# Optimization experiments

Measured on AMD Instinct MI355X. Metric: run time of the kernel, lower is better.

## Reference

```python
import jax, jax.numpy as jnp
import numpy as np

BT, P, C = 64, 1024, 1024   # bt = B*T with T=8 frames
T = 8
B = BT // T
RANK, DSTATE = 32, 16
SCALING = 128.0 / 32.0      # alpha / rank


def setup_inputs() -> dict:
    key = jax.random.key(0)
    ks = jax.random.split(key, 11)
    s = 0.02
    return {
        "x": jax.random.normal(ks[0], (BT, P, C), jnp.float32),
        "Wb": jax.random.normal(ks[1], (C, C), jnp.float32) * s,
        "bb": jax.random.normal(ks[2], (C,), jnp.float32) * s,
        "Wdown": jax.random.normal(ks[3], (RANK, C), jnp.float32) * s,
        "Wup": jax.random.normal(ks[4], (C, RANK), jnp.float32) * s,
        "A_log": jax.random.normal(ks[5], (RANK, DSTATE), jnp.float32),
        "Dp": jax.random.normal(ks[6], (RANK,), jnp.float32),
        "Wxp": jax.random.normal(ks[7], (RANK + 2 * DSTATE, RANK), jnp.float32) * s,
        "bxp": jnp.zeros((RANK + 2 * DSTATE,), jnp.float32),
        "Wout": jax.random.normal(ks[8], (RANK, RANK), jnp.float32) * s,
        "bout": jnp.zeros((RANK,), jnp.float32),
    }


def _minimal_ssm(xseq, A_log, Dp, Wxp, bxp, Wout, bout):
    # xseq: (N, T, r) -> (N, T, r); serial recurrence over T via lax.scan.
    N, Tn, r = xseq.shape
    A = -jnp.exp(A_log)  # (r, s)

    def step(h, x_t):  # h: (N, r, s), x_t: (N, r)
        proj = x_t @ Wxp.T + bxp                      # (N, r + 2s)
        dlt = jax.nn.softplus(proj[:, :r])            # (N, r)
        Bm = proj[:, r:r + DSTATE]                    # (N, s)
        Cm = proj[:, r + DSTATE:]                     # (N, s)
        A_bar = jnp.exp(dlt[:, :, None] * A)          # (N, r, s)
        B_bar = dlt[:, :, None] * Bm[:, None, :]      # (N, r, s)
        h = A_bar * h + B_bar * x_t[:, :, None]
        y = jnp.einsum('nrs,ns->nr', h, Cm) + Dp * x_t
        return h, y

    h0 = jnp.zeros((N, r, DSTATE), xseq.dtype)
    _, ys = jax.lax.scan(step, h0, jnp.swapaxes(xseq, 0, 1))  # ys: (T, N, r)
    out = jnp.swapaxes(ys, 0, 1)                               # (N, T, r)
    return out @ Wout.T + bout


def reference(x, Wb, bb, Wdown, Wup, A_log, Dp, Wxp, bxp, Wout, bout):
    base_out = x @ Wb.T + bb                                   # (BT, P, C)
    x_btpc = x.reshape(B, T, P, C)
    red = jnp.einsum('btpc,rc->btpr', x_btpc, Wdown)           # (B, T, P, r)
    red_seq = jnp.transpose(red, (0, 2, 1, 3)).reshape(B * P, T, RANK)
    red_seq = _minimal_ssm(red_seq, A_log, Dp, Wxp, bxp, Wout, bout)
    red_seq = jnp.transpose(red_seq.reshape(B, P, T, RANK), (0, 2, 1, 3))
    delta = jnp.einsum('btpr,cr->btpc', red_seq, Wup) * SCALING
    return base_out + delta.reshape(BT, P, C)
```

## Files before the change

### kernel.cpp

```cpp
#include <hip/hip_runtime.h>
#include <stdint.h>

typedef unsigned short u16;
typedef short short8 __attribute__((ext_vector_type(8)));
typedef float f32x4 __attribute__((ext_vector_type(4)));

#define MFMA16(a,b,c) __builtin_amdgcn_mfma_f32_16x16x32_bf16((a),(b),(c),0,0,0)

__device__ __forceinline__ u16 f2bf(float f) {
  union { float f; unsigned u; } v; v.f = f;
  unsigned r = v.u + 0x7FFFu + ((v.u >> 16) & 1u);
  return (u16)(r >> 16);
}

__device__ __forceinline__ void async16(u16* lds, const u16* g) {
  __builtin_amdgcn_global_load_lds(
      (const __attribute__((address_space(1))) void*)g,
      (__attribute__((address_space(3))) void*)lds, 16, 0, 0);
}

__global__ __launch_bounds__(256) void k_conv_w(const float* __restrict__ wb,
                                                const float* __restrict__ wdown,
                                                const float* __restrict__ wup,
                                                u16* __restrict__ wbb,
                                                u16* __restrict__ wdownb,
                                                u16* __restrict__ wupb) {
  int idx = blockIdx.x * blockDim.x + threadIdx.x;
  int total = gridDim.x * blockDim.x;
  for (int i = idx; i < 1024 * 1024 / 8; i += total) {
    const float4* p = (const float4*)(wb + (size_t)i * 8);
    float4 a = p[0], b = p[1];
    union { u16 h[8]; uint4 v; } o;
    o.h[0] = f2bf(a.x); o.h[1] = f2bf(a.y); o.h[2] = f2bf(a.z); o.h[3] = f2bf(a.w);
    o.h[4] = f2bf(b.x); o.h[5] = f2bf(b.y); o.h[6] = f2bf(b.z); o.h[7] = f2bf(b.w);
    *(uint4*)(wbb + (size_t)i * 8) = o.v;
  }
  for (int i = idx; i < 32 * 1024; i += total) wdownb[i] = f2bf(wdown[i]);
  for (int i = idx; i < 1024 * 32; i += total) wupb[i] = f2bf(wup[i] * 4.0f);
}

__global__ __launch_bounds__(256) void k_prep(const float* __restrict__ x,
                                              const u16* __restrict__ wdownb,
                                              u16* __restrict__ xb,
                                              float* __restrict__ red) {
  int lane = threadIdx.x & 63, wid = threadIdx.x >> 6;
  int base = blockIdx.x * 64 + wid * 16;
  int row = base + (lane & 15);
  int q8 = (lane >> 4) * 8;
  const float* gx = x + (size_t)row * 1024 + q8;
  u16* gxb = xb + (size_t)row * 1024 + q8;
  const u16* wd0 = wdownb + (size_t)(lane & 15) * 1024 + q8;
  f32x4 acc0 = {}, acc1 = {};
#pragma unroll 4
  for (int k0 = 0; k0 < 1024; k0 += 32) {
    float4 a = *(const float4*)(gx + k0);
    float4 c = *(const float4*)(gx + k0 + 4);
    union { u16 h[8]; uint4 v; short8 s; } o;
    o.h[0] = f2bf(a.x); o.h[1] = f2bf(a.y); o.h[2] = f2bf(a.z); o.h[3] = f2bf(a.w);
    o.h[4] = f2bf(c.x); o.h[5] = f2bf(c.y); o.h[6] = f2bf(c.z); o.h[7] = f2bf(c.w);
    *(uint4*)(gxb + k0) = o.v;
    short8 b0 = *(const short8*)(wd0 + k0);
    short8 b1 = *(const short8*)(wd0 + k0 + 16 * 1024);
    acc0 = MFMA16(o.s, b0, acc0);
    acc1 = MFMA16(o.s, b1, acc1);
  }
  int orow = base + (lane >> 4) * 4;
#pragma unroll
  for (int rr = 0; rr < 4; ++rr) {
    red[(size_t)(orow + rr) * 32 + (lane & 15)] = acc0[rr];
    red[(size_t)(orow + rr) * 32 + 16 + (lane & 15)] = acc1[rr];
  }
}

__global__ __launch_bounds__(256) void k_ssm(const float* __restrict__ red,
                                             u16* __restrict__ oseq,
                                             const float* __restrict__ A_log,
                                             const float* __restrict__ Dp,
                                             const float* __restrict__ Wxp,
                                             const float* __restrict__ bxp,
                                             const float* __restrict__ Wout,
                                             const float* __restrict__ bout) {
  int lane = threadIdx.x & 63;
  int r = lane & 31;
  int hb = lane & 32;
  int gw = blockIdx.x * 4 + (threadIdx.x >> 6);
  int n = gw * 2 + (lane >> 5);
  int b = n >> 10, p = n & 1023;
  float wxA[32], wxB[32], wo[32];
#pragma unroll
  for (int k = 0; k < 32; ++k) {
    wxA[k] = Wxp[r * 32 + k];
    wxB[k] = Wxp[(32 + r) * 32 + k];
    wo[k]  = Wout[r * 32 + k];
  }
  float Ar[16];
#pragma unroll
  for (int s = 0; s < 16; ++s) Ar[s] = -__expf(A_log[r * 16 + s]);
  float dpr = Dp[r];
  float bx1 = bxp[r], bx2 = bxp[32 + r], bo = bout[r];
  float h[16];
#pragma unroll
  for (int s = 0; s < 16; ++s) h[s] = 0.f;
  for (int t = 0; t < 8; ++t) {
    size_t rowt = (size_t)(b * 8 + t) * 1024 + p;
    float xr = red[rowt * 32 + r];
    float p1 = bx1, p2 = bx2;
#pragma unroll
    for (int k = 0; k < 32; ++k) {
      float xv = __shfl(xr, hb + k);
      p1 = fmaf(wxA[k], xv, p1);
      p2 = fmaf(wxB[k], xv, p2);
    }
    float dlt = (p1 > 20.f) ? p1 : log1pf(__expf(p1));
    float yr = dpr * xr;
#pragma unroll
    for (int s = 0; s < 16; ++s) {
      float Bm = __shfl(p2, hb + s);
      float Cm = __shfl(p2, hb + 16 + s);
      float ab = __expf(dlt * Ar[s]);
      h[s] = fmaf(ab, h[s], dlt * Bm * xr);
      yr = fmaf(h[s], Cm, yr);
    }
    float ov = bo;
#pragma unroll
    for (int k = 0; k < 32; ++k) ov = fmaf(wo[k], __shfl(yr, hb + k), ov);
    oseq[rowt * 32 + r] = f2bf(ov);
  }
}

__global__ __launch_bounds__(256) void k_gemm(const u16* __restrict__ xb,
                                              const u16* __restrict__ wbb,
                                              const u16* __restrict__ oseq,
                                              const u16* __restrict__ wupb,
                                              const float* __restrict__ bb,
                                              float* __restrict__ out) {
  __shared__ u16 As[128 * 32];
  __shared__ u16 Bs[128 * 32];
  int bid = blockIdx.x;
  int sw = (bid & 7) * 512 + (bid >> 3);
  int mt = sw >> 3, nt = sw & 7;
  int m0 = mt * 128, n0 = nt * 128;
  int tid = threadIdx.x, lane = tid & 63, wid = tid >> 6;
  int wr = (wid >> 1) * 64, wc = (wid & 1) * 64;
  f32x4 acc[4][4] = {};
  int srow = wid * 32 + (lane >> 2);
  int scol = (lane & 3) * 8;
  const u16* gA = xb  + (size_t)(m0 + srow) * 1024 + scol;
  const u16* gB = wbb + (size_t)(n0 + srow) * 1024 + scol;
  u16* lA = &As[wid * 32 * 32];
  u16* lB = &Bs[wid * 32 * 32];
  for (int k0 = 0; k0 < 1024; k0 += 32) {
    if (k0) __syncthreads();
    async16(lA,           gA + k0);
    async16(lA + 16 * 32, gA + k0 + (size_t)16 * 1024);
    async16(lB,           gB + k0);
    async16(lB + 16 * 32, gB + k0 + (size_t)16 * 1024);
    __syncthreads();
    short8 a[4], b[4];
#pragma unroll
    for (int mi = 0; mi < 4; ++mi)
      a[mi] = *(const short8*)&As[(wr + mi * 16 + (lane & 15)) * 32 + (lane >> 4) * 8];
#pragma unroll
    for (int ni = 0; ni < 4; ++ni)
      b[ni] = *(const short8*)&Bs[(wc + ni * 16 + (lane & 15)) * 32 + (lane >> 4) * 8];
#pragma unroll
    for (int mi = 0; mi < 4; ++mi)
#pragma unroll
      for (int ni = 0; ni < 4; ++ni)
        acc[mi][ni] = MFMA16(a[mi], b[ni], acc[mi][ni]);
  }
  short8 ae[4], be[4];
#pragma unroll
  for (int mi = 0; mi < 4; ++mi) {
    int row = m0 + wr + mi * 16 + (lane & 15);
    ae[mi] = *(const short8*)(oseq + (size_t)row * 32 + (lane >> 4) * 8);
  }
#pragma unroll
  for (int ni = 0; ni < 4; ++ni) {
    int col = n0 + wc + ni * 16 + (lane & 15);
    be[ni] = *(const short8*)(wupb + (size_t)col * 32 + (lane >> 4) * 8);
  }
#pragma unroll
  for (int mi = 0; mi < 4; ++mi)
#pragma unroll
    for (int ni = 0; ni < 4; ++ni)
      acc[mi][ni] = MFMA16(ae[mi], be[ni], acc[mi][ni]);
  float bias[4];
#pragma unroll
  for (int ni = 0; ni < 4; ++ni) bias[ni] = bb[n0 + wc + ni * 16 + (lane & 15)];
#pragma unroll
  for (int mi = 0; mi < 4; ++mi)
#pragma unroll
    for (int ni = 0; ni < 4; ++ni) {
      int col = n0 + wc + ni * 16 + (lane & 15);
#pragma unroll
      for (int r = 0; r < 4; ++r) {
        int row = m0 + wr + mi * 16 + (lane >> 4) * 4 + r;
        out[(size_t)row * 1024 + col] = acc[mi][ni][r] + bias[ni];
      }
    }
}

extern "C" void kernel_launch(void* const* d_in, const int* in_sizes, int n_in,
                              void* d_out, int out_size, void* d_ws, size_t ws_size,
                              hipStream_t stream) {
  const float* x     = (const float*)d_in[0];
  const float* Wb    = (const float*)d_in[1];
  const float* bb    = (const float*)d_in[2];
  const float* Wdown = (const float*)d_in[3];
  const float* Wup   = (const float*)d_in[4];
  const float* A_log = (const float*)d_in[5];
  const float* Dp    = (const float*)d_in[6];
  const float* Wxp   = (const float*)d_in[7];
  const float* bxp   = (const float*)d_in[8];
  const float* Wout  = (const float*)d_in[9];
  const float* bout  = (const float*)d_in[10];

  char* ws = (char*)d_ws;
  u16*   xb     = (u16*)(ws);
  u16*   wbb    = (u16*)(ws + 134217728);
  u16*   wdownb = (u16*)(ws + 136314880);
  u16*   wupb   = (u16*)(ws + 136380416);
  float* red    = (float*)(ws + 136445952);
  u16*   oseq   = (u16*)(ws + 144834560);
  float* out = (float*)d_out;

  hipLaunchKernelGGL(k_conv_w, dim3(512), dim3(256), 0, stream, Wb, Wdown, Wup, wbb, wdownb, wupb);
  hipLaunchKernelGGL(k_prep, dim3(1024), dim3(256), 0, stream, x, wdownb, xb, red);
  hipLaunchKernelGGL(k_ssm, dim3(1024), dim3(256), 0, stream, red, oseq, A_log, Dp, Wxp, bxp, Wout, bout);
  hipLaunchKernelGGL(k_gemm, dim3(4096), dim3(256), 0, stream, xb, wbb, oseq, wupb, bb, out);
}
```

Baseline: 686.7 us.

## Rewrite main GEMM with 256x256 tiles, double-buffered swizzled LDS pipeline

Replaces the 128x128 single-buffered GEMM with a 512-thread kernel computing 256x256 output tiles over K-steps of 64. It uses a double-buffered LDS with XOR swizzling and interleaves staged async global-to-LDS loads with MFMA phases under explicit waitcnt, barriers and priority hints. The aim is more data reuse per LDS byte, fewer bank conflicts, and hiding global load latency behind compute. In exchange it needs 128KB of dynamic LDS, which limits occupancy, and it depends on hand-tuned scheduling.

```diff
diff --git a/kernel.cpp b/kernel.cpp
--- a/kernel.cpp
+++ b/kernel.cpp
@@ -18,6 +18,11 @@
       (const __attribute__((address_space(1))) void*)g,
       (__attribute__((address_space(3))) void*)lds, 16, 0, 0);
 }
+
+#define LGKM0 do { asm volatile("s_waitcnt lgkmcnt(0)" ::: "memory"); \
+                   __builtin_amdgcn_sched_barrier(0); } while (0)
+#define BARR  do { __builtin_amdgcn_s_barrier(); \
+                   __builtin_amdgcn_sched_barrier(0); } while (0)
 
 __global__ __launch_bounds__(256) void k_conv_w(const float* __restrict__ wb,
                                                 const float* __restrict__ wdown,
@@ -128,77 +133,175 @@
   }
 }
 
-__global__ __launch_bounds__(256) void k_gemm(const u16* __restrict__ xb,
-                                              const u16* __restrict__ wbb,
-                                              const u16* __restrict__ oseq,
-                                              const u16* __restrict__ wupb,
-                                              const float* __restrict__ bb,
-                                              float* __restrict__ out) {
-  __shared__ u16 As[128 * 32];
-  __shared__ u16 Bs[128 * 32];
+__global__ __launch_bounds__(512, 2) void k_gemm2(const u16* __restrict__ xb,
+                                                  const u16* __restrict__ wbb,
+                                                  const u16* __restrict__ oseq,
+                                                  const u16* __restrict__ wupb,
+                                                  const float* __restrict__ bb,
+                                                  float* __restrict__ out) {
+  extern __shared__ u16 sm[];
   int bid = blockIdx.x;
-  int sw = (bid & 7) * 512 + (bid >> 3);
-  int mt = sw >> 3, nt = sw & 7;
-  int m0 = mt * 128, n0 = nt * 128;
-  int tid = threadIdx.x, lane = tid & 63, wid = tid >> 6;
-  int wr = (wid >> 1) * 64, wc = (wid & 1) * 64;
-  f32x4 acc[4][4] = {};
-  int srow = wid * 32 + (lane >> 2);
-  int scol = (lane & 3) * 8;
-  const u16* gA = xb  + (size_t)(m0 + srow) * 1024 + scol;
-  const u16* gB = wbb + (size_t)(n0 + srow) * 1024 + scol;
-  u16* lA = &As[wid * 32 * 32];
-  u16* lB = &Bs[wid * 32 * 32];
-  for (int k0 = 0; k0 < 1024; k0 += 32) {
-    if (k0) __syncthreads();
-    async16(lA,           gA + k0);
-    async16(lA + 16 * 32, gA + k0 + (size_t)16 * 1024);
-    async16(lB,           gB + k0);
-    async16(lB + 16 * 32, gB + k0 + (size_t)16 * 1024);
-    __syncthreads();
-    short8 a[4], b[4];
+  int swz = (bid & 7) * 128 + (bid >> 3);
+  int mt = swz >> 2, nt = swz & 3;
+  int m0 = mt * 256, n0 = nt * 256;
+  int tid = threadIdx.x;
+  int l = tid & 63, w = tid >> 6;
+  int wm = w >> 2, wn = w & 3;
+  int g = l >> 4, l15 = l & 15, l7 = l & 7, l3 = l >> 3;
+  int offk0 = (g ^ l7) * 8;
+  int offk1 = ((g + 4) ^ l7) * 8;
+  int ar[8], brr[4], rAnl[8], rBl[4];
+#pragma unroll
+  for (int mi = 0; mi < 8; ++mi) {
+    int rm = (mi < 4) ? (wm * 64 + mi * 16) : (128 + wm * 64 + (mi - 4) * 16);
+    rAnl[mi] = rm;
+    ar[mi] = (rm + l15) * 64;
+  }
+#pragma unroll
+  for (int nj = 0; nj < 4; ++nj) {
+    int rn = (nj < 2) ? (wn * 32 + nj * 16) : (128 + wn * 32 + (nj - 2) * 16);
+    rBl[nj] = rn + l15;
+    brr[nj] = 16384 + (rn + l15) * 64;
+  }
+  int slotg = l7 ^ l3;
+  const u16* pA[4];
+  const u16* pB[4];
+#pragma unroll
+  for (int j = 0; j < 4; ++j) {
+    pA[j] = xb  + (size_t)(m0 + (j * 8 + w) * 8 + l3) * 1024 + slotg * 8;
+    pB[j] = wbb + (size_t)(n0 + (j * 8 + w) * 8 + l3) * 1024 + slotg * 8;
+  }
+#pragma unroll
+  for (int j = 0; j < 4; ++j) async16(sm + (j * 8 + w) * 512, pA[j]);
+#pragma unroll
+  for (int j = 0; j < 4; ++j) async16(sm + 16384 + (j * 8 + w) * 512, pB[j]);
+#pragma unroll
+  for (int j = 0; j < 4; ++j) async16(sm + 32768 + (j * 8 + w) * 512, pA[j] + 64);
+#pragma unroll
+  for (int j = 0; j < 4; ++j) async16(sm + 32768 + 16384 + (j * 8 + w) * 512, pB[j] + 64);
+#pragma unroll
+  for (int j = 0; j < 4; ++j) { pA[j] += 128; pB[j] += 128; }
+  f32x4 acc[8][4] = {};
+  asm volatile("s_waitcnt vmcnt(8)" ::: "memory");
+  __builtin_amdgcn_sched_barrier(0);
+  BARR;
+  short8 af[4][2], bq[4][2];
+  for (int T = 0; T < 16; ++T) {
+    int sb = (T & 1) * 32768;
+    const u16* SA = sm + sb;
+    u16* stg = sm + sb;
+#pragma unroll
+    for (int mi = 0; mi < 4; ++mi) {
+      af[mi][0] = *(const short8*)(SA + ar[mi] + offk0);
+      af[mi][1] = *(const short8*)(SA + ar[mi] + offk1);
+    }
+#pragma unroll
+    for (int nj = 0; nj < 2; ++nj) {
+      bq[nj][0] = *(const short8*)(SA + brr[nj] + offk0);
+      bq[nj][1] = *(const short8*)(SA + brr[nj] + offk1);
+    }
+    LGKM0;
+    BARR;
+    if (T < 14) {
+      async16(stg + (0 * 8 + w) * 512, pA[0]);
+      async16(stg + (1 * 8 + w) * 512, pA[1]);
+      async16(stg + 16384 + (0 * 8 + w) * 512, pB[0]);
+      async16(stg + 16384 + (1 * 8 + w) * 512, pB[1]);
+    }
+    __builtin_amdgcn_sched_barrier(0);
+    __builtin_amdgcn_s_setprio(1);
 #pragma unroll
     for (int mi = 0; mi < 4; ++mi)
-      a[mi] = *(const short8*)&As[(wr + mi * 16 + (lane & 15)) * 32 + (lane >> 4) * 8];
-#pragma unroll
-    for (int ni = 0; ni < 4; ++ni)
-      b[ni] = *(const short8*)&Bs[(wc + ni * 16 + (lane & 15)) * 32 + (lane >> 4) * 8];
+#pragma unroll
+      for (int nj = 0; nj < 2; ++nj) {
+        acc[mi][nj] = MFMA16(af[mi][0], bq[nj][0], acc[mi][nj]);
+        acc[mi][nj] = MFMA16(af[mi][1], bq[nj][1], acc[mi][nj]);
+      }
+    __builtin_amdgcn_s_setprio(0);
+#pragma unroll
+    for (int nj = 2; nj < 4; ++nj) {
+      bq[nj][0] = *(const short8*)(SA + brr[nj] + offk0);
+      bq[nj][1] = *(const short8*)(SA + brr[nj] + offk1);
+    }
+    LGKM0;
+    BARR;
+    if (T < 14) {
+      async16(stg + 16384 + (2 * 8 + w) * 512, pB[2]);
+      async16(stg + 16384 + (3 * 8 + w) * 512, pB[3]);
+    }
+    __builtin_amdgcn_sched_barrier(0);
+    __builtin_amdgcn_s_setprio(1);
 #pragma unroll
     for (int mi = 0; mi < 4; ++mi)
 #pragma unroll
-      for (int ni = 0; ni < 4; ++ni)
-        acc[mi][ni] = MFMA16(a[mi], b[ni], acc[mi][ni]);
-  }
-  short8 ae[4], be[4];
-#pragma unroll
-  for (int mi = 0; mi < 4; ++mi) {
-    int row = m0 + wr + mi * 16 + (lane & 15);
-    ae[mi] = *(const short8*)(oseq + (size_t)row * 32 + (lane >> 4) * 8);
-  }
-#pragma unroll
-  for (int ni = 0; ni < 4; ++ni) {
-    int col = n0 + wc + ni * 16 + (lane & 15);
-    be[ni] = *(const short8*)(wupb + (size_t)col * 32 + (lane >> 4) * 8);
-  }
-#pragma unroll
-  for (int mi = 0; mi < 4; ++mi)
-#pragma unroll
-    for (int ni = 0; ni < 4; ++ni)
-      acc[mi][ni] = MFMA16(ae[mi], be[ni], acc[mi][ni]);
+      for (int nj = 2; nj < 4; ++nj) {
+        acc[mi][nj] = MFMA16(af[mi][0], bq[nj][0], acc[mi][nj]);
+        acc[mi][nj] = MFMA16(af[mi][1], bq[nj][1], acc[mi][nj]);
+      }
+    __builtin_amdgcn_s_setprio(0);
+#pragma unroll
+    for (int mi = 0; mi < 4; ++mi) {
+      af[mi][0] = *(const short8*)(SA + ar[4 + mi] + offk0);
+      af[mi][1] = *(const short8*)(SA + ar[4 + mi] + offk1);
+    }
+    LGKM0;
+    BARR;
+    if (T < 14) {
+      async16(stg + (2 * 8 + w) * 512, pA[2]);
+      async16(stg + (3 * 8 + w) * 512, pA[3]);
+    }
+    __builtin_amdgcn_sched_barrier(0);
+    __builtin_amdgcn_s_setprio(1);
+#pragma unroll
+    for (int mi = 0; mi < 4; ++mi)
+#pragma unroll
+      for (int nj = 0; nj < 2; ++nj) {
+        acc[4 + mi][nj] = MFMA16(af[mi][0], bq[nj][0], acc[4 + mi][nj]);
+        acc[4 + mi][nj] = MFMA16(af[mi][1], bq[nj][1], acc[4 + mi][nj]);
+      }
+    __builtin_amdgcn_s_setprio(0);
+    if (T < 14) {
+      asm volatile("s_waitcnt vmcnt(8)" ::: "memory");
+    } else {
+      asm volatile("s_waitcnt vmcnt(0)" ::: "memory");
+    }
+    __builtin_amdgcn_sched_barrier(0);
+    BARR;
+    __builtin_amdgcn_s_setprio(1);
+#pragma unroll
+    for (int mi = 0; mi < 4; ++mi)
+#pragma unroll
+      for (int nj = 2; nj < 4; ++nj) {
+        acc[4 + mi][nj] = MFMA16(af[mi][0], bq[nj][0], acc[4 + mi][nj]);
+        acc[4 + mi][nj] = MFMA16(af[mi][1], bq[nj][1], acc[4 + mi][nj]);
+      }
+    __builtin_amdgcn_s_setprio(0);
+#pragma unroll
+    for (int j = 0; j < 4; ++j) { pA[j] += 64; pB[j] += 64; }
+  }
+  short8 aeq[8], beq[4];
+#pragma unroll
+  for (int mi = 0; mi < 8; ++mi)
+    aeq[mi] = *(const short8*)(oseq + (size_t)(m0 + rAnl[mi] + l15) * 32 + g * 8);
+#pragma unroll
+  for (int nj = 0; nj < 4; ++nj)
+    beq[nj] = *(const short8*)(wupb + (size_t)(n0 + rBl[nj]) * 32 + g * 8);
+#pragma unroll
+  for (int mi = 0; mi < 8; ++mi)
+#pragma unroll
+    for (int nj = 0; nj < 4; ++nj)
+      acc[mi][nj] = MFMA16(aeq[mi], beq[nj], acc[mi][nj]);
   float bias[4];
 #pragma unroll
-  for (int ni = 0; ni < 4; ++ni) bias[ni] = bb[n0 + wc + ni * 16 + (lane & 15)];
-#pragma unroll
-  for (int mi = 0; mi < 4; ++mi)
-#pragma unroll
-    for (int ni = 0; ni < 4; ++ni) {
-      int col = n0 + wc + ni * 16 + (lane & 15);
-#pragma unroll
-      for (int r = 0; r < 4; ++r) {
-        int row = m0 + wr + mi * 16 + (lane >> 4) * 4 + r;
-        out[(size_t)row * 1024 + col] = acc[mi][ni][r] + bias[ni];
-      }
-    }
+  for (int nj = 0; nj < 4; ++nj) bias[nj] = bb[n0 + rBl[nj]];
+#pragma unroll
+  for (int mi = 0; mi < 8; ++mi)
+#pragma unroll
+    for (int nj = 0; nj < 4; ++nj)
+#pragma unroll
+      for (int r = 0; r < 4; ++r)
+        out[(size_t)(m0 + rAnl[mi] + g * 4 + r) * 1024 + n0 + rBl[nj]] =
+            acc[mi][nj][r] + bias[nj];
 }
 
 extern "C" void kernel_launch(void* const* d_in, const int* in_sizes, int n_in,
@@ -225,8 +328,11 @@
   u16*   oseq   = (u16*)(ws + 144834560);
   float* out = (float*)d_out;
 
+  hipFuncSetAttribute((const void*)k_gemm2,
+                      hipFuncAttributeMaxDynamicSharedMemorySize, 131072);
+
   hipLaunchKernelGGL(k_conv_w, dim3(512), dim3(256), 0, stream, Wb, Wdown, Wup, wbb, wdownb, wupb);
   hipLaunchKernelGGL(k_prep, dim3(1024), dim3(256), 0, stream, x, wdownb, xb, red);
   hipLaunchKernelGGL(k_ssm, dim3(1024), dim3(256), 0, stream, red, oseq, A_log, Dp, Wxp, bxp, Wout, bout);
-  hipLaunchKernelGGL(k_gemm, dim3(4096), dim3(256), 0, stream, xb, wbb, oseq, wupb, bb, out);
-}
+  hipLaunchKernelGGL(k_gemm2, dim3(1024), dim3(512), 131072, stream, xb, wbb, oseq, wupb, bb, out);
+}
```

After: 660.4 us. 3.8% less time.
